# Optimization experiments

Measured on AMD Instinct MI355X. Metric: run time of the kernel, lower is better.

The kernel has to match this reference:

```python
import jax, jax.numpy as jnp
import numpy as np

EPS = 1e-9
PI = 3.141592653589793


def _ciou_elementwise(b1, b2):
    """Elementwise CIoU between xyxy boxes b1, b2 of shape [..., 4].
    Mathematically identical to calculate_iou(b1, b2, 'ciou').diag() of the
    pairwise version, but O(N) instead of O(N^2)."""
    x1a, y1a, x2a, y2a = b1[..., 0], b1[..., 1], b1[..., 2], b1[..., 3]
    x1b, y1b, x2b, y2b = b2[..., 0], b2[..., 1], b2[..., 2], b2[..., 3]

    xmin = jnp.maximum(x1a, x1b)
    ymin = jnp.maximum(y1a, y1b)
    xmax = jnp.minimum(x2a, x2b)
    ymax = jnp.minimum(y2a, y2b)
    inter = jnp.clip(xmax - xmin, 0.0) * jnp.clip(ymax - ymin, 0.0)

    area1 = (x2a - x1a) * (y2a - y1a)
    area2 = (x2b - x1b) * (y2b - y1b)
    union = area1 + area2 - inter
    iou = inter / (union + EPS)

    # center distance
    cd = ((x1a + x2a) - (x1b + x2b)) ** 2 / 4.0 + ((y1a + y2a) - (y1b + y2b)) ** 2 / 4.0
    # enclosing box diagonal
    cw = jnp.maximum(x2a, x2b) - jnp.minimum(x1a, x1b)
    ch = jnp.maximum(y2a, y2b) - jnp.minimum(y1a, y1b)
    diag = cw ** 2 + ch ** 2 + EPS
    diou = iou - cd / diag

    # aspect-ratio consistency term
    at = jnp.arctan((x2a - x1a) / (y2a - y1a + EPS)) - jnp.arctan((x2b - x1b) / (y2b - y1b + EPS))
    v = (4.0 / PI ** 2) * at ** 2
    alpha = v / (v - iou + 1.0 + EPS)
    return diou - alpha * v


def setup_inputs() -> dict:
    key = jax.random.key(0)
    kp1, kp2, kt1, kt2, km = jax.random.split(key, 5)
    B, A = 64, 65536

    def make_boxes(kc, kw):
        cxy = jax.random.uniform(kc, (B, A, 2), jnp.float32, 0.0, 640.0)
        wh = jax.random.uniform(kw, (B, A, 2), jnp.float32, 1.0, 100.0)
        return jnp.concatenate([cxy - wh / 2.0, cxy + wh / 2.0], axis=-1)

    predicts_bbox = make_boxes(kp1, kp2)
    targets_bbox = make_boxes(kt1, kt2)
    valid_masks = jax.random.uniform(km, (B, A)) < 0.5
    return {
        "predicts_bbox": predicts_bbox,
        "targets_bbox": targets_bbox,
        "valid_masks": valid_masks,
        "box_norm": jnp.ones((1,), jnp.float32),
        "cls_norm": jnp.ones((1,), jnp.float32),
    }


def reference(predicts_bbox, targets_bbox, valid_masks, box_norm, cls_norm):
    # box_norm / cls_norm are unused by the original forward.
    iou = _ciou_elementwise(predicts_bbox, targets_bbox)  # [B, A]
    m = valid_masks.astype(iou.dtype)
    n_valid = jnp.maximum(jnp.sum(m), 1.0)
    loss_iou = jnp.sum((1.0 - iou) * m) / n_valid  # mean over valid entries
    # original returns the gathered iou vector; we return the full masked map
    # (iou at valid positions, 0 elsewhere) to stay jit-compatible.
    return (loss_iou, iou * m)
```

## Files before the change

kernel.cpp:

```cpp
#include <hip/hip_runtime.h>


constexpr float EPSF      = 1e-9f;
constexpr float HALF_PI_F = 1.5707963267948966f;
constexpr float INV_PI2_4 = 0.40528473456935109f;

__device__ __forceinline__ float fast_rcp(float x) { return __builtin_amdgcn_rcpf(x); }

__device__ __forceinline__ float fast_atan(float t) {
    float a = fabsf(t);
    bool big = a > 1.0f;
    float x = big ? fast_rcp(a) : a;
    float s = x * x;
    float p = -0.0117212f;
    p = fmaf(p, s, 0.05265332f);
    p = fmaf(p, s, -0.11643287f);
    p = fmaf(p, s, 0.19354346f);
    p = fmaf(p, s, -0.33262347f);
    p = fmaf(p, s, 0.99997726f);
    p = x * p;
    float r = big ? (HALF_PI_F - p) : p;
    return copysignf(r, t);
}

__device__ __forceinline__ float ciou_one(float x1a, float y1a, float x2a, float y2a,
                                          float x1b, float y1b, float x2b, float y2b) {
    float xmin = fmaxf(x1a, x1b), ymin = fmaxf(y1a, y1b);
    float xmax = fminf(x2a, x2b), ymax = fminf(y2a, y2b);
    float inter = fmaxf(xmax - xmin, 0.0f) * fmaxf(ymax - ymin, 0.0f);
    float wa = x2a - x1a, ha = y2a - y1a;
    float wb = x2b - x1b, hb = y2b - y1b;
    float uni = wa * ha + wb * hb - inter;
    float iou = inter * fast_rcp(uni + EPSF);
    float dx = (x1a + x2a) - (x1b + x2b);
    float dy = (y1a + y2a) - (y1b + y2b);
    float cd = 0.25f * (dx * dx + dy * dy);
    float cw = fmaxf(x2a, x2b) - fminf(x1a, x1b);
    float ch = fmaxf(y2a, y2b) - fminf(y1a, y1b);
    float diag = cw * cw + ch * ch + EPSF;
    float ha_ = ha + EPSF, hb_ = hb + EPSF;
    float at = fast_atan((wa * hb_ - wb * ha_) * fast_rcp(ha_ * hb_ + wa * wb + EPSF));
    float v = INV_PI2_4 * at * at;
    float av = v * v * fast_rcp(v - iou + 1.0f + EPSF);
    return iou - cd * fast_rcp(diag) - av;
}

__global__ __launch_bounds__(256) void ciou_main(const float4* __restrict__ pred4,
                                                 const float4* __restrict__ targ4,
                                                 const int* __restrict__ mask,
                                                 float* __restrict__ out, int n,
                                                 float* __restrict__ part_loss,
                                                 float* __restrict__ part_cnt) {
    const int i = threadIdx.x;
    float lsum = 0.0f;
    int cnt = 0;

    for (int base = blockIdx.x * 1024; base < n; base += gridDim.x * 1024) {
        if (base + 1024 <= n) {
            float4 p[4], q[4];
            int m[4];
            #pragma unroll
            for (int k = 0; k < 4; ++k) p[k] = pred4[base + 256 * k + i];
            #pragma unroll
            for (int k = 0; k < 4; ++k) q[k] = targ4[base + 256 * k + i];
            #pragma unroll
            for (int k = 0; k < 4; ++k) m[k] = mask[base + 256 * k + i];
            #pragma unroll
            for (int k = 0; k < 4; ++k) {
                bool valid = m[k] != 0;
                float mf = valid ? 1.0f : 0.0f;
                float c = ciou_one(p[k].x, p[k].y, p[k].z, p[k].w,
                                   q[k].x, q[k].y, q[k].z, q[k].w);
                out[1 + base + 256 * k + i] = c * mf;
                lsum += (1.0f - c) * mf;
                cnt += valid ? 1 : 0;
            }
        } else {
            #pragma unroll
            for (int k = 0; k < 4; ++k) {
                int b = base + 256 * k + i;
                if (b < n) {
                    float4 p = pred4[b], q = targ4[b];
                    bool valid = mask[b] != 0;
                    float mf = valid ? 1.0f : 0.0f;
                    float c = ciou_one(p.x, p.y, p.z, p.w, q.x, q.y, q.z, q.w);
                    out[1 + b] = c * mf;
                    lsum += (1.0f - c) * mf;
                    cnt += valid ? 1 : 0;
                }
            }
        }
    }

    for (int off = 32; off > 0; off >>= 1) {
        lsum += __shfl_down(lsum, off);
        cnt  += __shfl_down(cnt, off);
    }
    __shared__ float sl[4];
    __shared__ int   sc[4];
    int w = threadIdx.x >> 6, lane = threadIdx.x & 63;
    if (lane == 0) { sl[w] = lsum; sc[w] = cnt; }
    __syncthreads();
    if (threadIdx.x == 0) {
        part_loss[blockIdx.x] = sl[0] + sl[1] + sl[2] + sl[3];
        part_cnt[blockIdx.x]  = (float)(sc[0] + sc[1] + sc[2] + sc[3]);
    }
}

__global__ __launch_bounds__(1024) void finalize_kernel(const float* __restrict__ part_loss,
                                                        const float* __restrict__ part_cnt,
                                                        float* __restrict__ out, int nb) {
    __shared__ double sl[1024], sc[1024];
    const int t = threadIdx.x;
    double l = 0.0, c = 0.0;
    for (int j = t; j < nb; j += 1024) {
        l += (double)part_loss[j];
        c += (double)part_cnt[j];
    }
    sl[t] = l; sc[t] = c;
    __syncthreads();
    for (int s = 512; s > 0; s >>= 1) {
        if (t < s) { sl[t] += sl[t + s]; sc[t] += sc[t + s]; }
        __syncthreads();
    }
    if (t == 0) out[0] = (float)(sl[0] / fmax(sc[0], 1.0));
}

extern "C" void kernel_launch(void* const* d_in, const int* in_sizes, int n_in,
                              void* d_out, int out_size, void* d_ws, size_t ws_size,
                              hipStream_t stream) {
    const float4* pred4 = (const float4*)d_in[0];
    const float4* targ4 = (const float4*)d_in[1];
    const int*    mask  = (const int*)d_in[2];
    float* out = (float*)d_out;
    int n = in_sizes[0] / 4;

    int nblocks = (n + 1023) / 1024;
    int ws_cap = (int)(ws_size / (2 * sizeof(float)));
    if (nblocks > ws_cap) nblocks = ws_cap;
    if (nblocks > 8192) nblocks = 8192;
    if (nblocks < 1) nblocks = 1;
    float* part_loss = (float*)d_ws;
    float* part_cnt  = part_loss + nblocks;

    ciou_main<<<nblocks, 256, 0, stream>>>(pred4, targ4, mask, out, n, part_loss, part_cnt);
    finalize_kernel<<<1, 1024, 0, stream>>>(part_loss, part_cnt, out, nblocks);
}
```

Before: 33.91 us.

## Stage inputs through LDS with direct global-to-LDS loads, halve per-block chunk

Replaces the per-thread register loads of pred/target boxes and the mask with global_load_lds DMA copies into shared memory, followed by a barrier and reads from LDS. The per-iteration chunk drops from 1024 to 512 elements and the grid sizing is adjusted to match. The aim is to cut VGPR pressure and use the direct-to-LDS load path. In exchange it adds two block barriers per iteration and serialises load then compute, with no double buffering. The nblocks cap of 8192 now covers fewer elements per grid pass, so each block loops more times.

```diff
diff --git a/kernel.cpp b/kernel.cpp
--- a/kernel.cpp
+++ b/kernel.cpp
@@ -6,6 +6,15 @@
 constexpr float INV_PI2_4 = 0.40528473456935109f;
 
 __device__ __forceinline__ float fast_rcp(float x) { return __builtin_amdgcn_rcpf(x); }
+
+__device__ __forceinline__ void glds16(const void* g, void* l) {
+    __builtin_amdgcn_global_load_lds((const __attribute__((address_space(1))) void*)g,
+                                     (__attribute__((address_space(3))) void*)l, 16, 0, 0);
+}
+__device__ __forceinline__ void glds4(const void* g, void* l) {
+    __builtin_amdgcn_global_load_lds((const __attribute__((address_space(1))) void*)g,
+                                     (__attribute__((address_space(3))) void*)l, 4, 0, 0);
+}
 
 __device__ __forceinline__ float fast_atan(float t) {
     float a = fabsf(t);
@@ -51,33 +60,42 @@
                                                  float* __restrict__ out, int n,
                                                  float* __restrict__ part_loss,
                                                  float* __restrict__ part_cnt) {
+    __shared__ float4 spred[512];
+    __shared__ float4 starg[512];
+    __shared__ int    smask[512];
+
     const int i = threadIdx.x;
+    const int w = i >> 6, l = i & 63;
     float lsum = 0.0f;
     int cnt = 0;
 
-    for (int base = blockIdx.x * 1024; base < n; base += gridDim.x * 1024) {
-        if (base + 1024 <= n) {
-            float4 p[4], q[4];
-            int m[4];
+    for (int base = blockIdx.x * 512; base < n; base += gridDim.x * 512) {
+        if (base + 512 <= n) {
+            const int c0 = 2 * w, c1 = c0 + 1;
+            glds16(pred4 + base + 64 * c0 + l, &spred[64 * c0]);
+            glds16(pred4 + base + 64 * c1 + l, &spred[64 * c1]);
+            glds16(targ4 + base + 64 * c0 + l, &starg[64 * c0]);
+            glds16(targ4 + base + 64 * c1 + l, &starg[64 * c1]);
+            glds4 (mask  + base + 64 * c0 + l, &smask[64 * c0]);
+            glds4 (mask  + base + 64 * c1 + l, &smask[64 * c1]);
+            __syncthreads();
+
             #pragma unroll
-            for (int k = 0; k < 4; ++k) p[k] = pred4[base + 256 * k + i];
-            #pragma unroll
-            for (int k = 0; k < 4; ++k) q[k] = targ4[base + 256 * k + i];
-            #pragma unroll
-            for (int k = 0; k < 4; ++k) m[k] = mask[base + 256 * k + i];
-            #pragma unroll
-            for (int k = 0; k < 4; ++k) {
-                bool valid = m[k] != 0;
+            for (int k = 0; k < 2; ++k) {
+                const int t = 256 * k + i;
+                float4 p = spred[t];
+                float4 q = starg[t];
+                bool valid = smask[t] != 0;
                 float mf = valid ? 1.0f : 0.0f;
-                float c = ciou_one(p[k].x, p[k].y, p[k].z, p[k].w,
-                                   q[k].x, q[k].y, q[k].z, q[k].w);
-                out[1 + base + 256 * k + i] = c * mf;
+                float c = ciou_one(p.x, p.y, p.z, p.w, q.x, q.y, q.z, q.w);
+                out[1 + base + t] = c * mf;
                 lsum += (1.0f - c) * mf;
                 cnt += valid ? 1 : 0;
             }
+            __syncthreads();
         } else {
             #pragma unroll
-            for (int k = 0; k < 4; ++k) {
+            for (int k = 0; k < 2; ++k) {
                 int b = base + 256 * k + i;
                 if (b < n) {
                     float4 p = pred4[b], q = targ4[b];
@@ -98,10 +116,9 @@
     }
     __shared__ float sl[4];
     __shared__ int   sc[4];
-    int w = threadIdx.x >> 6, lane = threadIdx.x & 63;
-    if (lane == 0) { sl[w] = lsum; sc[w] = cnt; }
+    if ((i & 63) == 0) { sl[w] = lsum; sc[w] = cnt; }
     __syncthreads();
-    if (threadIdx.x == 0) {
+    if (i == 0) {
         part_loss[blockIdx.x] = sl[0] + sl[1] + sl[2] + sl[3];
         part_cnt[blockIdx.x]  = (float)(sc[0] + sc[1] + sc[2] + sc[3]);
     }
@@ -135,7 +152,7 @@
     float* out = (float*)d_out;
     int n = in_sizes[0] / 4;
 
-    int nblocks = (n + 1023) / 1024;
+    int nblocks = (n + 511) / 512;
     int ws_cap = (int)(ws_size / (2 * sizeof(float)));
     if (nblocks > ws_cap) nblocks = ws_cap;
     if (nblocks > 8192) nblocks = 8192;
```

After: 34.99 us. 1.03x slower.
